# Performance work log

Hardware: AMD Instinct MI355X
Metric: run time of the kernel (lower is better)

## Reference

```python
import jax, jax.numpy as jnp
import numpy as np

KS = 3
N = KS * KS
LN_EPS = 1e-5


def conv2d(x, w, stride=1, pad=0):
    return jax.lax.conv_general_dilated(
        x, w, (stride, stride), [(pad, pad), (pad, pad)],
        dimension_numbers=('NCHW', 'OIHW', 'NCHW'))


def layer_norm(x, g, b):
    mu = jnp.mean(x, axis=-1, keepdims=True)
    var = jnp.mean(jnp.square(x - mu), axis=-1, keepdims=True)
    return (x - mu) * jax.lax.rsqrt(var + LN_EPS) * g + b


def l2norm(x):
    n = jnp.sqrt(jnp.sum(jnp.square(x), axis=-1, keepdims=True))
    return x / jnp.maximum(n, 1e-12)


def deform_conv(x, w_p, b_p, w_d):
    # canonical DeformConv2d (kernel 3, pad 1, stride 1, no modulation)
    B, C, H, W = x.shape
    off = conv2d(x, w_p, stride=1, pad=1) + b_p[None, :, None, None]  # [B,2N,H,W]
    xp = jnp.pad(x, ((0, 0), (0, 0), (1, 1), (1, 1)))
    Hp, Wp = H + 2, W + 2
    pn = jnp.stack(jnp.meshgrid(jnp.arange(-1, 2), jnp.arange(-1, 2), indexing='ij'), 0)
    pn = pn.reshape(2, N).astype(x.dtype)  # kernel offsets, row-major (dx,dy)
    p0x = jnp.arange(1, H + 1, dtype=x.dtype)
    p0y = jnp.arange(1, W + 1, dtype=x.dtype)
    # sampling coords, [B,H,W,N]
    px = off[:, :N].transpose(0, 2, 3, 1) + p0x[None, :, None, None] + pn[0][None, None, None, :]
    py = off[:, N:].transpose(0, 2, 3, 1) + p0y[None, None, :, None] + pn[1][None, None, None, :]
    fx = jnp.floor(px)
    fy = jnp.floor(py)
    qlx = jnp.clip(fx, 0, Hp - 1)
    qly = jnp.clip(fy, 0, Wp - 1)
    qrx = jnp.clip(fx + 1, 0, Hp - 1)
    qry = jnp.clip(fy + 1, 0, Wp - 1)
    pxc = jnp.clip(px, 0, Hp - 1)
    pyc = jnp.clip(py, 0, Wp - 1)
    g_lt = (1 + (qlx - pxc)) * (1 + (qly - pyc))
    g_rb = (1 - (qrx - pxc)) * (1 - (qry - pyc))
    g_lb = (1 + (qlx - pxc)) * (1 - (qry - pyc))
    g_rt = (1 - (qrx - pxc)) * (1 + (qly - pyc))
    xf = xp.reshape(B, C, Hp * Wp)

    def gat(ix, iy):
        idx = (ix.astype(jnp.int32) * Wp + iy.astype(jnp.int32)).reshape(B, 1, -1)
        g = jnp.take_along_axis(xf, jnp.broadcast_to(idx, (B, C, idx.shape[-1])), axis=2)
        return g.reshape(B, C, H, W, N)

    xo = (g_lt[:, None] * gat(qlx, qly) + g_rb[:, None] * gat(qrx, qry)
          + g_lb[:, None] * gat(qlx, qry) + g_rt[:, None] * gat(qrx, qly))
    # [B,C,H,W,N] -> [B,C,H*ks,W*ks] (row = h*ks+kr, col = w*ks+kc)
    xo = xo.reshape(B, C, H, W, KS, KS).transpose(0, 1, 2, 4, 3, 5).reshape(B, C, H * KS, W * KS)
    return conv2d(xo, w_d, stride=KS, pad=0)


def setup_inputs() -> dict:
    key = jax.random.key(0)
    ks = jax.random.split(key, 8)
    B, C, H, W, heads = 4, 192, 64, 64, 6
    hid = 4 * C
    return {
        'x': jax.random.normal(ks[0], (B, C, H, W), dtype=jnp.float32),
        'gamma1': jnp.ones((C,), jnp.float32),
        'beta1': jnp.zeros((C,), jnp.float32),
        'gamma2': jnp.ones((C,), jnp.float32),
        'beta2': jnp.zeros((C,), jnp.float32),
        'temperature': jnp.ones((heads, 1, 1), jnp.float32),
        'w_qkv': jax.random.normal(ks[1], (3 * C, C), jnp.float32) * 0.02,
        'w_proj': jax.random.normal(ks[2], (C, C), jnp.float32) * 0.02,
        'w_p': jax.random.normal(ks[3], (2 * N, C, KS, KS), jnp.float32) * 0.01,
        'b_p': jnp.zeros((2 * N,), jnp.float32),
        'w_d': jax.random.normal(ks[4], (C, C, KS, KS), jnp.float32) * 0.02,
        'w_fc1': jax.random.normal(ks[5], (C, hid), jnp.float32) * 0.02,
        'b_fc1': jnp.zeros((hid,), jnp.float32),
        'w_fc2': jax.random.normal(ks[6], (hid, C), jnp.float32) * 0.02,
        'b_fc2': jnp.zeros((C,), jnp.float32),
    }


def reference(x, gamma1, beta1, gamma2, beta2, temperature, w_qkv, w_proj,
              w_p, b_p, w_d, w_fc1, b_fc1, w_fc2, b_fc2):
    B, C, H, W = x.shape
    heads = temperature.shape[0]
    xs = x.reshape(B, C, H * W).transpose(0, 2, 1)  # [B,HW,C]
    shortcut = xs
    xn = layer_norm(xs, gamma1, beta1).transpose(0, 2, 1).reshape(B, C, H, W)
    # SSA: deformable-conv query + channel attention over C
    q = deform_conv(xn, w_p, b_p, w_d)
    qkv = jnp.einsum('bchw,oc->bohw', xn, w_qkv)
    k_spe, v_spe = qkv[:, C:2 * C], qkv[:, 2 * C:]

    def split(t):
        return t.reshape(B, heads, C // heads, H * W)

    qh = split(q)
    kh = l2norm(split(k_spe))
    vh = l2norm(split(v_spe))
    attn = jnp.einsum('bhcn,bhdn->bhcd', qh, kh) * temperature[None]
    attn = jax.nn.softmax(attn, axis=-1)
    out = jnp.einsum('bhcd,bhdn->bhcn', attn, vh).reshape(B, C, H, W)
    out = jnp.einsum('bchw,oc->bohw', out, w_proj)
    xs2 = shortcut + out.reshape(B, C, H * W).transpose(0, 2, 1)
    h1 = layer_norm(xs2, gamma2, beta2)
    m = jax.nn.gelu(h1 @ w_fc1 + b_fc1, approximate=False) @ w_fc2 + b_fc2
    xs3 = xs2 + m
    return xs3.transpose(0, 2, 1).reshape(B, C, H, W)
```

## Files before the change

### kernel.cpp

```cpp
#include <hip/hip_runtime.h>
#include <math.h>

typedef unsigned short u16;
typedef unsigned int u32;
typedef short s16x8 __attribute__((ext_vector_type(8)));
typedef float f32x4 __attribute__((ext_vector_type(4)));

#define AS1 __attribute__((address_space(1)))
#define AS3 __attribute__((address_space(3)))

__device__ __forceinline__ float bf2f(u16 u) {
    union { u32 i; float f; } v; v.i = ((u32)u) << 16; return v.f;
}
__device__ __forceinline__ u16 f2bf(float f) {
    union { float f; u32 i; } v; v.f = f;
    u32 r = v.i + 0x7fffu + ((v.i >> 16) & 1u);
    return (u16)(r >> 16);
}
__device__ __forceinline__ void gll16(const u16* g, u16* l) {
    __builtin_amdgcn_global_load_lds((const AS1 u32*)g, (AS3 u32*)l, 16, 0, 0);
}

__global__ void prep_kernel(const float* __restrict__ wd, const float* __restrict__ wqkv,
                            const float* __restrict__ wfc1, const float* __restrict__ wfc2,
                            const float* __restrict__ wp,
                            u16* __restrict__ wdT, u16* __restrict__ wkvT,
                            u16* __restrict__ wf1T, u16* __restrict__ wf2T,
                            u16* __restrict__ wpT)
{
    int i = blockIdx.x * 256 + threadIdx.x;
    if (i < 331776) {
        int o = i / 1728, r = i % 1728;
        int p = r / 192, c = r % 192;
        wdT[i] = f2bf(wd[(o * 192 + c) * 9 + p]);
    }
    if (i < 73728) {
        int o = i / 192, c = i % 192;
        wkvT[i] = f2bf(wqkv[(192 + o) * 192 + c]);
    }
    if (i < 147456) {
        int n = i / 192, c = i % 192;
        wf1T[i] = f2bf(wfc1[c * 768 + n]);
        int n2 = i / 768, hh = i % 768;
        wf2T[i] = f2bf(wfc2[hh * 192 + n2]);
    }
    if (i < 31104) {
        int n = i / 1728, r = i % 1728;
        int p = r / 192, c = r % 192;
        wpT[i] = f2bf(wp[(n * 192 + c) * 9 + p]);
    } else if (i < 55296) {
        wpT[i] = 0;
    }
}

__global__ __launch_bounds__(256) void ln1_kernel(const float* __restrict__ x,
                                                  const float* __restrict__ g,
                                                  const float* __restrict__ be,
                                                  u16* __restrict__ xn)
{
    __shared__ float red0[256], red1[256];
    __shared__ float mu_s[64], rs_s[64];
    __shared__ u16 tile[64 * 194];
    int t = threadIdx.x, tl = t & 63, cg = t >> 6;
    int m0 = blockIdx.x * 64;
    int b = m0 >> 12, hw0 = m0 & 4095;
    const float* xb = x + (size_t)b * 786432 + hw0 + tl;
    float s = 0.f, s2 = 0.f;
    for (int cc = cg; cc < 192; cc += 4) { float v = xb[cc * 4096]; s += v; s2 += v * v; }
    red0[t] = s; red1[t] = s2;
    __syncthreads();
    if (t < 64) {
        float a = red0[t] + red0[64 + t] + red0[128 + t] + red0[192 + t];
        float q = red1[t] + red1[64 + t] + red1[128 + t] + red1[192 + t];
        float mu = a * (1.f / 192.f);
        float var = q * (1.f / 192.f) - mu * mu;
        mu_s[t] = mu; rs_s[t] = rsqrtf(var + 1e-5f);
    }
    __syncthreads();
    float mu = mu_s[tl], rs = rs_s[tl];
    for (int cc = cg; cc < 192; cc += 4) {
        float v = (xb[cc * 4096] - mu) * rs * g[cc] + be[cc];
        tile[tl * 194 + cc] = f2bf(v);
    }
    __syncthreads();
    u32* dst = (u32*)(xn + (size_t)m0 * 192);
    for (int i = t; i < 64 * 96; i += 256) {
        int r = i / 96, c2 = i % 96;
        dst[i] = *(const u32*)&tile[r * 194 + c2 * 2];
    }
}

__global__ __launch_bounds__(256) void offconv_kernel(const u16* __restrict__ xn,
                                                      const u16* __restrict__ wpT,
                                                      const float* __restrict__ bp,
                                                      float* __restrict__ off)
{
    __shared__ u16 As[64 * 200];
    __shared__ u16 Bs[32 * 200];
    int bh = blockIdx.x;
    int b = bh >> 6, h = bh & 63;
    int t = threadIdx.x;
    int lane = t & 63, wv = t >> 6;
    f32x4 acc[2];
#pragma unroll
    for (int j = 0; j < 2; j++) { acc[j][0] = 0.f; acc[j][1] = 0.f; acc[j][2] = 0.f; acc[j][3] = 0.f; }
    int r = t >> 2, cq = (t & 3) * 48;
    for (int p = 0; p < 9; p++) {
        int dh = p / 3 - 1, dw = p % 3 - 1;
        int hr = h + dh, wr = r + dw;
        bool valid = (hr >= 0) && (hr < 64) && (wr >= 0) && (wr < 64);
        const u16* src = xn + ((size_t)(b * 4096 + hr * 64 + wr)) * 192 + cq;
#pragma unroll
        for (int j = 0; j < 6; j++) {
            s16x8 v = {0, 0, 0, 0, 0, 0, 0, 0};
            if (valid) v = *(const s16x8*)(src + j * 8);
            *(s16x8*)&As[r * 200 + cq + j * 8] = v;
        }
#pragma unroll
        for (int i = 0; i < 3; i++) {
            int q = t + i * 256;
            int n = q / 24, c8 = q % 24;
            *(s16x8*)&Bs[n * 200 + c8 * 8] =
                *(const s16x8*)(wpT + n * 1728 + p * 192 + c8 * 8);
        }
        __syncthreads();
#pragma unroll
        for (int kc = 0; kc < 6; kc++) {
            s16x8 af = *(const s16x8*)&As[(wv * 16 + (lane & 15)) * 200 + kc * 32 + (lane >> 4) * 8];
            s16x8 b0 = *(const s16x8*)&Bs[(lane & 15) * 200 + kc * 32 + (lane >> 4) * 8];
            s16x8 b1 = *(const s16x8*)&Bs[(16 + (lane & 15)) * 200 + kc * 32 + (lane >> 4) * 8];
            acc[0] = __builtin_amdgcn_mfma_f32_16x16x32_bf16(af, b0, acc[0], 0, 0, 0);
            acc[1] = __builtin_amdgcn_mfma_f32_16x16x32_bf16(af, b1, acc[1], 0, 0, 0);
        }
        __syncthreads();
    }
    int col = lane & 15;
    int wbase = wv * 16 + (lane >> 4) * 4;
#pragma unroll
    for (int j = 0; j < 2; j++) {
        int n = j * 16 + col;
        if (n < 18) {
            float bb = bp[n];
#pragma unroll
            for (int rr = 0; rr < 4; rr++) {
                int w = wbase + rr;
                off[((size_t)(b * 4096 + h * 64 + w)) * 18 + n] = acc[j][rr] + bb;
            }
        }
    }
}

__global__ __launch_bounds__(256) void gemm_deform(const u16* __restrict__ xn,
                                                   const float* __restrict__ off,
                                                   const u16* __restrict__ wdT,
                                                   u16* __restrict__ qt)
{
    __shared__ u16 As[2][32 * 200];
    __shared__ int sidx[32][9][4];
    __shared__ float swt[32][9][4];
    int t = threadIdx.x, lane = t & 63, wv = t >> 6;
    int m0 = blockIdx.x * 32;
    int b = m0 >> 12;
    for (int i = t; i < 288; i += 256) {
        int mi = i / 9, p = i % 9;
        int m = m0 + mi;
        int hw = m & 4095;
        int h = hw >> 6, w = hw & 63;
        float ox = off[(size_t)m * 18 + p];
        float oy = off[(size_t)m * 18 + 9 + p];
        float px = ox + (float)(h + 1) + (float)(p / 3 - 1);
        float py = oy + (float)(w + 1) + (float)(p % 3 - 1);
        float fx = floorf(px), fy = floorf(py);
        float qlx = fminf(fmaxf(fx, 0.f), 65.f);
        float qly = fminf(fmaxf(fy, 0.f), 65.f);
        float qrx = fminf(fmaxf(fx + 1.f, 0.f), 65.f);
        float qry = fminf(fmaxf(fy + 1.f, 0.f), 65.f);
        float pxc = fminf(fmaxf(px, 0.f), 65.f);
        float pyc = fminf(fmaxf(py, 0.f), 65.f);
        float gxl = 1.f + (qlx - pxc), gxr = 1.f - (qrx - pxc);
        float gyl = 1.f + (qly - pyc), gyr = 1.f - (qry - pyc);
        int xl = (int)qlx, xr = (int)qrx, yl = (int)qly, yr = (int)qry;
        int cx[4] = {xl, xr, xl, xr};
        int cy[4] = {yl, yr, yr, yl};
        float cw[4] = {gxl * gyl, gxr * gyr, gxl * gyr, gxr * gyl};
#pragma unroll
        for (int k = 0; k < 4; k++) {
            bool ok = (cx[k] >= 1) && (cx[k] <= 64) && (cy[k] >= 1) && (cy[k] <= 64);
            sidx[mi][p][k] = ok ? (b * 4096 + (cx[k] - 1) * 64 + (cy[k] - 1)) * 192 : 0;
            swt[mi][p][k] = ok ? cw[k] : 0.f;
        }
    }
    __syncthreads();
    f32x4 acc[2][3];
#pragma unroll
    for (int i = 0; i < 2; i++)
#pragma unroll
        for (int j = 0; j < 3; j++) {
            acc[i][j][0] = 0.f; acc[i][j][1] = 0.f; acc[i][j][2] = 0.f; acc[i][j][3] = 0.f;
        }
    int mi_[3], ch_[3];
#pragma unroll
    for (int u = 0; u < 3; u++) { int c = t + u * 256; mi_[u] = c / 24; ch_[u] = (c % 24) * 8; }

    {
        s16x8 pc[3][4];
#pragma unroll
        for (int u = 0; u < 3; u++) {
            const int* si = sidx[mi_[u]][0];
#pragma unroll
            for (int k = 0; k < 4; k++) pc[u][k] = *(const s16x8*)(xn + si[k] + ch_[u]);
        }
#pragma unroll
        for (int u = 0; u < 3; u++) {
            const float* sw = swt[mi_[u]][0];
            float v[8] = {0.f, 0.f, 0.f, 0.f, 0.f, 0.f, 0.f, 0.f};
#pragma unroll
            for (int k = 0; k < 4; k++) {
                float wt = sw[k];
#pragma unroll
                for (int j = 0; j < 8; j++) v[j] += wt * bf2f((u16)pc[u][k][j]);
            }
            s16x8 ov;
#pragma unroll
            for (int j = 0; j < 8; j++) ov[j] = (short)f2bf(v[j]);
            *(s16x8*)&As[0][mi_[u] * 200 + ch_[u]] = ov;
        }
    }
    __syncthreads();

    for (int p = 0; p < 9; p++) {
        int cur = p & 1;
        s16x8 nc[3][4];
        if (p < 8) {
#pragma unroll
            for (int u = 0; u < 3; u++) {
                const int* si = sidx[mi_[u]][p + 1];
#pragma unroll
                for (int k = 0; k < 4; k++) nc[u][k] = *(const s16x8*)(xn + si[k] + ch_[u]);
            }
        }
        const u16* wp_base = wdT + p * 192;
#pragma unroll
        for (int kk = 0; kk < 6; kk++) {
            s16x8 af[2], bfr[3];
#pragma unroll
            for (int i = 0; i < 2; i++)
                af[i] = *(const s16x8*)&As[cur][(i * 16 + (lane & 15)) * 200 + kk * 32 + (lane >> 4) * 8];
#pragma unroll
            for (int j = 0; j < 3; j++)
                bfr[j] = *(const s16x8*)(wp_base + (size_t)(wv * 48 + j * 16 + (lane & 15)) * 1728 + kk * 32 + (lane >> 4) * 8);
#pragma unroll
            for (int i = 0; i < 2; i++)
#pragma unroll
                for (int j = 0; j < 3; j++)
                    acc[i][j] = __builtin_amdgcn_mfma_f32_16x16x32_bf16(af[i], bfr[j], acc[i][j], 0, 0, 0);
        }
        if (p < 8) {
#pragma unroll
            for (int u = 0; u < 3; u++) {
                const float* sw = swt[mi_[u]][p + 1];
                float v[8] = {0.f, 0.f, 0.f, 0.f, 0.f, 0.f, 0.f, 0.f};
#pragma unroll
                for (int k = 0; k < 4; k++) {
                    float wt = sw[k];
#pragma unroll
                    for (int j = 0; j < 8; j++) v[j] += wt * bf2f((u16)nc[u][k][j]);
                }
                s16x8 ov;
#pragma unroll
                for (int j = 0; j < 8; j++) ov[j] = (short)f2bf(v[j]);
                *(s16x8*)&As[cur ^ 1][mi_[u] * 200 + ch_[u]] = ov;
            }
            __syncthreads();
        }
    }
    int col = lane & 15;
#pragma unroll
    for (int i = 0; i < 2; i++)
#pragma unroll
        for (int j = 0; j < 3; j++) {
            int mm = m0 + i * 16 + (lane >> 4) * 4;
            int nn = wv * 48 + j * 16 + col;
#pragma unroll
            for (int r = 0; r < 4; r++)
                qt[(size_t)(mm + r) * 192 + nn] = f2bf(acc[i][j][r]);
        }
}

template<int BM, int BN, int WM, int WN, int EP>
__global__ __launch_bounds__((BM / WM) * (BN / WN) * 64)
void gemm_bt(const u16* __restrict__ A, int lda,
             const u16* __restrict__ B, int ldb, int bstride,
             void* __restrict__ out, int ldc,
             const float* __restrict__ ex1, int K)
{
    constexpr int BK = 32;
    constexpr int WAVES_M = BM / WM, WAVES_N = BN / WN, NW = WAVES_M * WAVES_N;
    constexpr int TM = WM / 16, TN = WN / 16;
    constexpr int NLA = BM / 16, NLB = BN / 16;
    __shared__ u16 As[BM * BK];
    __shared__ u16 Bs[BN * BK];
    int tid = threadIdx.x;
    int lane = tid & 63, wv = tid >> 6;
    int wm = wv % WAVES_M, wn = wv / WAVES_M;
    int m0 = blockIdx.x * BM, n0 = blockIdx.y * BN;
    const u16* Bp = B + (size_t)(m0 >> 12) * bstride;
    f32x4 acc[TM][TN];
#pragma unroll
    for (int i = 0; i < TM; i++)
#pragma unroll
        for (int j = 0; j < TN; j++) {
            acc[i][j][0] = 0.f; acc[i][j][1] = 0.f; acc[i][j][2] = 0.f; acc[i][j][3] = 0.f;
        }
    int arow_l = lane >> 2;
    int acol_l = (lane & 3) * 8;
    for (int k0 = 0; k0 < K; k0 += BK) {
#pragma unroll 1
        for (int j = wv; j < NLA + NLB; j += NW) {
            if (j < NLA) {
                int row = j * 16 + arow_l;
                gll16(A + (size_t)(m0 + row) * lda + k0 + acol_l, As + j * 512);
            } else {
                int row = (j - NLA) * 16 + arow_l;
                gll16(Bp + (size_t)(n0 + row) * ldb + k0 + acol_l, Bs + (j - NLA) * 512);
            }
        }
        asm volatile("s_waitcnt vmcnt(0)" ::: "memory");
        __syncthreads();
        s16x8 af[TM], bfr[TN];
#pragma unroll
        for (int i = 0; i < TM; i++)
            af[i] = *(const s16x8*)&As[(wm * WM + i * 16 + (lane & 15)) * BK + (lane >> 4) * 8];
#pragma unroll
        for (int j = 0; j < TN; j++)
            bfr[j] = *(const s16x8*)&Bs[(wn * WN + j * 16 + (lane & 15)) * BK + (lane >> 4) * 8];
#pragma unroll
        for (int i = 0; i < TM; i++)
#pragma unroll
            for (int j = 0; j < TN; j++)
                acc[i][j] = __builtin_amdgcn_mfma_f32_16x16x32_bf16(af[i], bfr[j], acc[i][j], 0, 0, 0);
        __syncthreads();
    }
    int col = lane & 15;
#pragma unroll
    for (int i = 0; i < TM; i++)
#pragma unroll
        for (int j = 0; j < TN; j++) {
            int mm = m0 + wm * WM + i * 16 + (lane >> 4) * 4;
            int nn = n0 + wn * WN + j * 16 + col;
            if (EP == 0) {
                u16* o = (u16*)out;
#pragma unroll
                for (int r = 0; r < 4; r++) o[(size_t)(mm + r) * ldc + nn] = f2bf(acc[i][j][r]);
            } else if (EP == 1) {
                float* o = (float*)out;
                const float* xr = ex1 + (size_t)(mm >> 12) * 786432 + (size_t)nn * 4096 + (mm & 4095);
#pragma unroll
                for (int r = 0; r < 4; r++) o[(size_t)(mm + r) * ldc + nn] = acc[i][j][r] + xr[r];
            } else if (EP == 2) {
                u16* o = (u16*)out;
                float bb = ex1[nn];
#pragma unroll
                for (int r = 0; r < 4; r++) {
                    float v = acc[i][j][r] + bb;
                    o[(size_t)(mm + r) * ldc + nn] = f2bf(0.5f * v * (1.f + erff(v * 0.70710678118654752f)));
                }
            } else {
                float* o = (float*)out;
                float bb = ex1[nn];
#pragma unroll
                for (int r = 0; r < 4; r++) o[(size_t)(mm + r) * ldc + nn] = acc[i][j][r] + bb;
            }
        }
}

__global__ __launch_bounds__(384) void norm_kernel(const u16* __restrict__ kv,
                                                   float* __restrict__ norm2)
{
    int b = blockIdx.y, ch = blockIdx.x;
    int t = threadIdx.x;
    const u16* base = kv + ((size_t)(b * 4096 + ch * 128)) * 384 + t;
    float s = 0.f;
    for (int r = 0; r < 128; r++) { float v = bf2f(base[(size_t)r * 384]); s += v * v; }
    atomicAdd(&norm2[b * 384 + t], s);
}

__global__ __launch_bounds__(64) void attnp_kernel(const u16* __restrict__ qt,
                                                   const u16* __restrict__ kvt,
                                                   float* __restrict__ raw)
{
    __shared__ float qT[32 * 69];
    __shared__ float kT[32 * 69];
    int ch = blockIdx.x, h = blockIdx.y, b = blockIdx.z;
    int t = threadIdx.x;
    size_t base = (size_t)(b * 4096 + ch * 64);
    for (int e = t; e < 2048; e += 64) {
        int r = e >> 5, c = e & 31;
        qT[c * 69 + r] = bf2f(qt[(base + r) * 192 + h * 32 + c]);
        kT[c * 69 + r] = bf2f(kvt[(base + r) * 384 + h * 32 + c]);
    }
    __syncthreads();
    int tc = t >> 3, td = t & 7;
    int c0 = tc * 4, d0 = td * 4;
    float acc[4][4] = {};
    for (int r = 0; r < 64; r++) {
        float qv[4], kv4[4];
#pragma unroll
        for (int u = 0; u < 4; u++) { qv[u] = qT[(c0 + u) * 69 + r]; kv4[u] = kT[(d0 + u) * 69 + r]; }
#pragma unroll
        for (int u = 0; u < 4; u++)
#pragma unroll
            for (int v = 0; v < 4; v++) acc[u][v] += qv[u] * kv4[v];
    }
    float* dst = raw + ((size_t)(b * 6 + h)) * 1024;
#pragma unroll
    for (int u = 0; u < 4; u++)
#pragma unroll
        for (int v = 0; v < 4; v++)
            atomicAdd(&dst[(c0 + u) * 32 + d0 + v], acc[u][v]);
}

__global__ __launch_bounds__(1024) void softmax_kernel(const float* __restrict__ raw,
                                                       const float* __restrict__ norm2,
                                                       const float* __restrict__ temp,
                                                       float* __restrict__ att2)
{
    int h = blockIdx.x, b = blockIdx.y;
    int t = threadIdx.x;
    int c = t >> 5, d = t & 31;
    __shared__ float invk[32], invv[32];
    if (t < 32)       invk[t] = 1.f / fmaxf(sqrtf(norm2[b * 384 + h * 32 + t]), 1e-12f);
    else if (t < 64)  invv[t - 32] = 1.f / fmaxf(sqrtf(norm2[b * 384 + 192 + h * 32 + (t - 32)]), 1e-12f);
    __syncthreads();
    float T = temp[h];
    float v = raw[((size_t)(b * 6 + h) * 32 + c) * 32 + d] * invk[d] * T;
    float mx = v;
    for (int s = 16; s > 0; s >>= 1) mx = fmaxf(mx, __shfl_xor(mx, s, 32));
    float e = expf(v - mx);
    float sm = e;
    for (int s = 16; s > 0; s >>= 1) sm += __shfl_xor(sm, s, 32);
    att2[((size_t)(b * 6 + h) * 32 + c) * 32 + d] = (e / sm) * invv[d];
}

__global__ __launch_bounds__(192) void mb_kernel(const float* __restrict__ wproj,
                                                 const float* __restrict__ att2,
                                                 u16* __restrict__ Mb)
{
    int o2 = blockIdx.x, b = blockIdx.y, t = threadIdx.x;
    int h = t >> 5, d = t & 31;
    float s = 0.f;
#pragma unroll
    for (int c = 0; c < 32; c++)
        s += wproj[o2 * 192 + h * 32 + c] * att2[((size_t)(b * 6 + h) * 32 + c) * 32 + d];
    Mb[((size_t)b * 192 + o2) * 192 + t] = f2bf(s);
}

__global__ __launch_bounds__(256) void ln2_kernel(const float* __restrict__ xs2,
                                                  const float* __restrict__ g,
                                                  const float* __restrict__ be,
                                                  u16* __restrict__ h1)
{
    int t = threadIdx.x;
    int wv = t >> 6, l = t & 63;
    size_t m = (size_t)blockIdx.x * 4 + wv;
    const float* row = xs2 + m * 192;
    float v0 = row[l], v1 = row[l + 64], v2 = row[l + 128];
    float s = v0 + v1 + v2, s2 = v0 * v0 + v1 * v1 + v2 * v2;
    for (int sh = 32; sh > 0; sh >>= 1) { s += __shfl_xor(s, sh); s2 += __shfl_xor(s2, sh); }
    float mu = s * (1.f / 192.f);
    float var = s2 * (1.f / 192.f) - mu * mu;
    float rs = rsqrtf(var + 1e-5f);
    u16* o = h1 + m * 192;
    o[l]       = f2bf((v0 - mu) * rs * g[l]       + be[l]);
    o[l + 64]  = f2bf((v1 - mu) * rs * g[l + 64]  + be[l + 64]);
    o[l + 128] = f2bf((v2 - mu) * rs * g[l + 128] + be[l + 128]);
}

__global__ __launch_bounds__(256) void final_kernel(const float* __restrict__ xs2,
                                                    const float* __restrict__ m2,
                                                    float* __restrict__ out)
{
    __shared__ float tile[192 * 65];
    int blk = blockIdx.x;
    int b = blk >> 6, hw0 = (blk & 63) * 64;
    int t = threadIdx.x;
    size_t mbase = ((size_t)b * 4096 + hw0) * 192;
    for (int i = t; i < 64 * 192; i += 256) {
        int r = i / 192, c = i % 192;
        tile[c * 65 + r] = xs2[mbase + i] + m2[mbase + i];
    }
    __syncthreads();
    for (int i = t; i < 64 * 192; i += 256) {
        int c = i / 64, r = i % 64;
        out[(size_t)b * 786432 + (size_t)c * 4096 + hw0 + r] = tile[c * 65 + r];
    }
}

extern "C" void kernel_launch(void* const* d_in, const int* in_sizes, int n_in,
                              void* d_out, int out_size, void* d_ws, size_t ws_size,
                              hipStream_t stream)
{
    const float* x      = (const float*)d_in[0];
    const float* gamma1 = (const float*)d_in[1];
    const float* beta1  = (const float*)d_in[2];
    const float* gamma2 = (const float*)d_in[3];
    const float* beta2  = (const float*)d_in[4];
    const float* temp   = (const float*)d_in[5];
    const float* w_qkv  = (const float*)d_in[6];
    const float* w_proj = (const float*)d_in[7];
    const float* w_p    = (const float*)d_in[8];
    const float* b_p    = (const float*)d_in[9];
    const float* w_d    = (const float*)d_in[10];
    const float* w_fc1  = (const float*)d_in[11];
    const float* b_fc1  = (const float*)d_in[12];
    const float* w_fc2  = (const float*)d_in[13];
    const float* b_fc2  = (const float*)d_in[14];
    float* out = (float*)d_out;
    char* ws = (char*)d_ws;

    u16*   xn    = (u16*)(ws + 0);
    float* off   = (float*)(ws + 6291456);
    u16*   adef  = (u16*)(ws + 7471104);
    u16*   wpT   = adef;
    u16*   m1    = adef;
    float* m2    = (float*)(ws + 7471104 + 25165824);
    u16*   qt    = (u16*)(ws + 64094208);
    u16*   kvt   = (u16*)(ws + 70385664);
    float* norm2 = (float*)(ws + 82968576);
    float* araw  = (float*)(ws + 82974720);
    float* att2  = (float*)(ws + 83073024);
    u16*   Mb    = (u16*)(ws + 83171328);
    float* xs2   = (float*)(ws + 83318784);
    u16*   h1    = xn;
    u16*   wdT   = (u16*)(ws + 95901696);
    u16*   wkvT  = (u16*)(ws + 96565248);
    u16*   wf1T  = (u16*)(ws + 96712704);
    u16*   wf2T  = (u16*)(ws + 97007616);

    hipMemsetAsync(norm2, 0, 6144 + 98304, stream);
    prep_kernel<<<1296, 256, 0, stream>>>(w_d, w_qkv, w_fc1, w_fc2, w_p, wdT, wkvT, wf1T, wf2T, wpT);
    ln1_kernel<<<256, 256, 0, stream>>>(x, gamma1, beta1, xn);
    offconv_kernel<<<256, 256, 0, stream>>>(xn, wpT, b_p, off);
    gemm_deform<<<512, 256, 0, stream>>>(xn, off, wdT, qt);
    gemm_bt<128, 128, 64, 64, 0><<<dim3(128, 3), 256, 0, stream>>>(xn, 192, wkvT, 192, 0, kvt, 384, nullptr, 192);
    norm_kernel<<<dim3(32, 4), 384, 0, stream>>>(kvt, norm2);
    attnp_kernel<<<dim3(64, 6, 4), 64, 0, stream>>>(qt, kvt, araw);
    softmax_kernel<<<dim3(6, 4), 1024, 0, stream>>>(araw, norm2, temp, att2);
    mb_kernel<<<dim3(192, 4), 192, 0, stream>>>(w_proj, att2, Mb);
    gemm_bt<32, 192, 32, 96, 1><<<dim3(512, 1), 128, 0, stream>>>(kvt + 192, 384, Mb, 192, 192 * 192, xs2, 192, x, 192);
    ln2_kernel<<<4096, 256, 0, stream>>>(xs2, gamma2, beta2, h1);
    gemm_bt<128, 128, 64, 64, 2><<<dim3(128, 6), 256, 0, stream>>>(h1, 192, wf1T, 192, 0, m1, 768, b_fc1, 192);
    gemm_bt<32, 192, 32, 96, 3><<<dim3(512, 1), 128, 0, stream>>>(m1, 768, wf2T, 768, 0, m2, 192, b_fc2, 768);
    final_kernel<<<256, 256, 0, stream>>>(xs2, m2, out);
}
```

Before: 292.4 us.

## Double deform-GEMM block threads and split waves across M and N tiles

The deformable-conv GEMM kernel now runs 512 threads per block as 8 waves arranged 2x4 over M and N. Each wave computes a 16x48 tile instead of 32x48, and each thread gathers 12 channels of one sample point with 12-byte vector loads instead of three 8-channel chunks. The aim is more wave-level parallelism and fewer live registers per thread, to hide the latency of the scattered bilinear gathers. In exchange the same weight fragments are loaded from global memory by twice as many waves, and the 12-byte loads are less aligned.

```diff
diff --git a/kernel.cpp b/kernel.cpp
--- a/kernel.cpp
+++ b/kernel.cpp
@@ -5,12 +5,19 @@
 typedef unsigned int u32;
 typedef short s16x8 __attribute__((ext_vector_type(8)));
 typedef float f32x4 __attribute__((ext_vector_type(4)));
+typedef u32 u32x3 __attribute__((ext_vector_type(3)));
 
 #define AS1 __attribute__((address_space(1)))
 #define AS3 __attribute__((address_space(3)))
 
 __device__ __forceinline__ float bf2f(u16 u) {
     union { u32 i; float f; } v; v.i = ((u32)u) << 16; return v.f;
+}
+__device__ __forceinline__ float bflo(u32 u) {
+    union { u32 i; float f; } v; v.i = u << 16; return v.f;
+}
+__device__ __forceinline__ float bfhi(u32 u) {
+    union { u32 i; float f; } v; v.i = u & 0xffff0000u; return v.f;
 }
 __device__ __forceinline__ u16 f2bf(float f) {
     union { float f; u32 i; } v; v.f = f;
@@ -150,18 +157,19 @@
     }
 }
 
-__global__ __launch_bounds__(256) void gemm_deform(const u16* __restrict__ xn,
-                                                   const float* __restrict__ off,
-                                                   const u16* __restrict__ wdT,
-                                                   u16* __restrict__ qt)
+__global__ __launch_bounds__(512, 4) void gemm_deform(const u16* __restrict__ xn,
+                                                      const float* __restrict__ off,
+                                                      const u16* __restrict__ wdT,
+                                                      u16* __restrict__ qt)
 {
     __shared__ u16 As[2][32 * 200];
     __shared__ int sidx[32][9][4];
     __shared__ float swt[32][9][4];
     int t = threadIdx.x, lane = t & 63, wv = t >> 6;
+    int wm = wv & 1, wn = wv >> 1;
     int m0 = blockIdx.x * 32;
     int b = m0 >> 12;
-    for (int i = t; i < 288; i += 256) {
+    for (int i = t; i < 288; i += 512) {
         int mi = i / 9, p = i % 9;
         int m = m0 + mi;
         int hw = m & 4095;
@@ -191,100 +199,96 @@
         }
     }
     __syncthreads();
-    f32x4 acc[2][3];
-#pragma unroll
-    for (int i = 0; i < 2; i++)
-#pragma unroll
-        for (int j = 0; j < 3; j++) {
-            acc[i][j][0] = 0.f; acc[i][j][1] = 0.f; acc[i][j][2] = 0.f; acc[i][j][3] = 0.f;
-        }
-    int mi_[3], ch_[3];
-#pragma unroll
-    for (int u = 0; u < 3; u++) { int c = t + u * 256; mi_[u] = c / 24; ch_[u] = (c % 24) * 8; }
+    f32x4 acc[3];
+#pragma unroll
+    for (int j = 0; j < 3; j++) { acc[j][0] = 0.f; acc[j][1] = 0.f; acc[j][2] = 0.f; acc[j][3] = 0.f; }
+    int mi = t >> 4, ch = (t & 15) * 12;
 
     {
-        s16x8 pc[3][4];
-#pragma unroll
-        for (int u = 0; u < 3; u++) {
-            const int* si = sidx[mi_[u]][0];
-#pragma unroll
-            for (int k = 0; k < 4; k++) pc[u][k] = *(const s16x8*)(xn + si[k] + ch_[u]);
-        }
-#pragma unroll
-        for (int u = 0; u < 3; u++) {
-            const float* sw = swt[mi_[u]][0];
-            float v[8] = {0.f, 0.f, 0.f, 0.f, 0.f, 0.f, 0.f, 0.f};
+        const int*   si = sidx[mi][0];
+        const float* sw = swt[mi][0];
+        float v[12];
+#pragma unroll
+        for (int j = 0; j < 12; j++) v[j] = 0.f;
+#pragma unroll
+        for (int k = 0; k < 4; k++) {
+            u32x3 a = *(const u32x3*)(xn + si[k] + ch);
+            u32x3 c2 = *(const u32x3*)(xn + si[k] + ch + 6);
+            float wt = sw[k];
+#pragma unroll
+            for (int j = 0; j < 3; j++) {
+                v[2 * j]     += wt * bflo(a[j]);
+                v[2 * j + 1] += wt * bfhi(a[j]);
+                v[6 + 2 * j]     += wt * bflo(c2[j]);
+                v[6 + 2 * j + 1] += wt * bfhi(c2[j]);
+            }
+        }
+        u32 o[6];
+#pragma unroll
+        for (int j = 0; j < 6; j++)
+            o[j] = (u32)f2bf(v[2 * j]) | ((u32)f2bf(v[2 * j + 1]) << 16);
+        *(u32x3*)&As[0][mi * 200 + ch]     = u32x3{o[0], o[1], o[2]};
+        *(u32x3*)&As[0][mi * 200 + ch + 6] = u32x3{o[3], o[4], o[5]};
+    }
+    __syncthreads();
+
+    for (int p = 0; p < 9; p++) {
+        int cur = p & 1;
+        u32x3 na[4], nb[4];
+        if (p < 8) {
+            const int* si = sidx[mi][p + 1];
+#pragma unroll
+            for (int k = 0; k < 4; k++) {
+                na[k] = *(const u32x3*)(xn + si[k] + ch);
+                nb[k] = *(const u32x3*)(xn + si[k] + ch + 6);
+            }
+        }
+        const u16* wp_base = wdT + p * 192;
+#pragma unroll
+        for (int kk = 0; kk < 6; kk++) {
+            s16x8 af = *(const s16x8*)&As[cur][(wm * 16 + (lane & 15)) * 200 + kk * 32 + (lane >> 4) * 8];
+            s16x8 bfr[3];
+#pragma unroll
+            for (int j = 0; j < 3; j++)
+                bfr[j] = *(const s16x8*)(wp_base + (size_t)(wn * 48 + j * 16 + (lane & 15)) * 1728 + kk * 32 + (lane >> 4) * 8);
+#pragma unroll
+            for (int j = 0; j < 3; j++)
+                acc[j] = __builtin_amdgcn_mfma_f32_16x16x32_bf16(af, bfr[j], acc[j], 0, 0, 0);
+        }
+        if (p < 8) {
+            const float* sw = swt[mi][p + 1];
+            float v[12];
+#pragma unroll
+            for (int j = 0; j < 12; j++) v[j] = 0.f;
 #pragma unroll
             for (int k = 0; k < 4; k++) {
                 float wt = sw[k];
 #pragma unroll
-                for (int j = 0; j < 8; j++) v[j] += wt * bf2f((u16)pc[u][k][j]);
+                for (int j = 0; j < 3; j++) {
+                    v[2 * j]     += wt * bflo(na[k][j]);
+                    v[2 * j + 1] += wt * bfhi(na[k][j]);
+                    v[6 + 2 * j]     += wt * bflo(nb[k][j]);
+                    v[6 + 2 * j + 1] += wt * bfhi(nb[k][j]);
+                }
             }
-            s16x8 ov;
-#pragma unroll
-            for (int j = 0; j < 8; j++) ov[j] = (short)f2bf(v[j]);
-            *(s16x8*)&As[0][mi_[u] * 200 + ch_[u]] = ov;
-        }
-    }
-    __syncthreads();
-
-    for (int p = 0; p < 9; p++) {
-        int cur = p & 1;
-        s16x8 nc[3][4];
-        if (p < 8) {
-#pragma unroll
-            for (int u = 0; u < 3; u++) {
-                const int* si = sidx[mi_[u]][p + 1];
-#pragma unroll
-                for (int k = 0; k < 4; k++) nc[u][k] = *(const s16x8*)(xn + si[k] + ch_[u]);
-            }
-        }
-        const u16* wp_base = wdT + p * 192;
-#pragma unroll
-        for (int kk = 0; kk < 6; kk++) {
-            s16x8 af[2], bfr[3];
-#pragma unroll
-            for (int i = 0; i < 2; i++)
-                af[i] = *(const s16x8*)&As[cur][(i * 16 + (lane & 15)) * 200 + kk * 32 + (lane >> 4) * 8];
-#pragma unroll
-            for (int j = 0; j < 3; j++)
-                bfr[j] = *(const s16x8*)(wp_base + (size_t)(wv * 48 + j * 16 + (lane & 15)) * 1728 + kk * 32 + (lane >> 4) * 8);
-#pragma unroll
-            for (int i = 0; i < 2; i++)
-#pragma unroll
-                for (int j = 0; j < 3; j++)
-                    acc[i][j] = __builtin_amdgcn_mfma_f32_16x16x32_bf16(af[i], bfr[j], acc[i][j], 0, 0, 0);
-        }
-        if (p < 8) {
-#pragma unroll
-            for (int u = 0; u < 3; u++) {
-                const float* sw = swt[mi_[u]][p + 1];
-                float v[8] = {0.f, 0.f, 0.f, 0.f, 0.f, 0.f, 0.f, 0.f};
-#pragma unroll
-                for (int k = 0; k < 4; k++) {
-                    float wt = sw[k];
-#pragma unroll
-                    for (int j = 0; j < 8; j++) v[j] += wt * bf2f((u16)nc[u][k][j]);
-                }
-                s16x8 ov;
-#pragma unroll
-                for (int j = 0; j < 8; j++) ov[j] = (short)f2bf(v[j]);
-                *(s16x8*)&As[cur ^ 1][mi_[u] * 200 + ch_[u]] = ov;
-            }
+            u32 o[6];
+#pragma unroll
+            for (int j = 0; j < 6; j++)
+                o[j] = (u32)f2bf(v[2 * j]) | ((u32)f2bf(v[2 * j + 1]) << 16);
+            *(u32x3*)&As[cur ^ 1][mi * 200 + ch]     = u32x3{o[0], o[1], o[2]};
+            *(u32x3*)&As[cur ^ 1][mi * 200 + ch + 6] = u32x3{o[3], o[4], o[5]};
             __syncthreads();
         }
     }
     int col = lane & 15;
 #pragma unroll
-    for (int i = 0; i < 2; i++)
-#pragma unroll
-        for (int j = 0; j < 3; j++) {
-            int mm = m0 + i * 16 + (lane >> 4) * 4;
-            int nn = wv * 48 + j * 16 + col;
-#pragma unroll
-            for (int r = 0; r < 4; r++)
-                qt[(size_t)(mm + r) * 192 + nn] = f2bf(acc[i][j][r]);
-        }
+    for (int j = 0; j < 3; j++) {
+        int mm = m0 + wm * 16 + (lane >> 4) * 4;
+        int nn = wn * 48 + j * 16 + col;
+#pragma unroll
+        for (int r = 0; r < 4; r++)
+            qt[(size_t)(mm + r) * 192 + nn] = f2bf(acc[j][r]);
+    }
 }
 
 template<int BM, int BN, int WM, int WN, int EP>
@@ -541,7 +545,7 @@
     prep_kernel<<<1296, 256, 0, stream>>>(w_d, w_qkv, w_fc1, w_fc2, w_p, wdT, wkvT, wf1T, wf2T, wpT);
     ln1_kernel<<<256, 256, 0, stream>>>(x, gamma1, beta1, xn);
     offconv_kernel<<<256, 256, 0, stream>>>(xn, wpT, b_p, off);
-    gemm_deform<<<512, 256, 0, stream>>>(xn, off, wdT, qt);
+    gemm_deform<<<512, 512, 0, stream>>>(xn, off, wdT, qt);
     gemm_bt<128, 128, 64, 64, 0><<<dim3(128, 3), 256, 0, stream>>>(xn, 192, wkvT, 192, 0, kvt, 384, nullptr, 192);
     norm_kernel<<<dim3(32, 4), 384, 0, stream>>>(kvt, norm2);
     attnp_kernel<<<dim3(64, 6, 4), 64, 0, stream>>>(qt, kvt, araw);
```

Result: slower. 330.6 us (+13.0%).

## Stage deform-conv weight slices in swizzled LDS with a larger M tile

Applied to the files above, without the earlier changes.

The deform GEMM now works on 64-row tiles with 512 threads and 8 waves arranged 2x4. For each kernel tap it loads the full 192x192 weight slice into LDS via global_load_lds, in an XOR-swizzled layout produced by the prep kernel, so B fragments come from shared memory instead of strided global reads. The double-buffered A tile becomes a single buffer with an extra barrier. This cuts repeated global weight traffic per block but raises LDS use to about 100KB, which limits occupancy, and it serializes the weight load with compute.

```diff
diff --git a/kernel.cpp b/kernel.cpp
--- a/kernel.cpp
+++ b/kernel.cpp
@@ -32,7 +32,8 @@
     if (i < 331776) {
         int o = i / 1728, r = i % 1728;
         int p = r / 192, c = r % 192;
-        wdT[i] = f2bf(wd[(o * 192 + c) * 9 + p]);
+        int cs = c ^ ((o & 7) << 3);
+        wdT[(p * 192 + o) * 192 + cs] = f2bf(wd[(o * 192 + c) * 9 + p]);
     }
     if (i < 73728) {
         int o = i / 192, c = i % 192;
@@ -150,18 +151,20 @@
     }
 }
 
-__global__ __launch_bounds__(256) void gemm_deform(const u16* __restrict__ xn,
-                                                   const float* __restrict__ off,
-                                                   const u16* __restrict__ wdT,
-                                                   u16* __restrict__ qt)
-{
-    __shared__ u16 As[2][32 * 200];
-    __shared__ int sidx[32][9][4];
-    __shared__ float swt[32][9][4];
+__global__ __launch_bounds__(512, 2) void gemm_deform(const u16* __restrict__ xn,
+                                                      const float* __restrict__ off,
+                                                      const u16* __restrict__ wdT,
+                                                      u16* __restrict__ qt)
+{
+    __shared__ u16 As[64 * 200];
+    __shared__ u16 Bs[192 * 192];
+    __shared__ int sidx[64][9][4];
+    __shared__ float swt[64][9][4];
     int t = threadIdx.x, lane = t & 63, wv = t >> 6;
-    int m0 = blockIdx.x * 32;
+    int wm = wv & 1, wn = wv >> 1;
+    int m0 = blockIdx.x * 64;
     int b = m0 >> 12;
-    for (int i = t; i < 288; i += 256) {
+    for (int i = t; i < 576; i += 512) {
         int mi = i / 9, p = i % 9;
         int m = m0 + mi;
         int hw = m & 4095;
@@ -198,79 +201,103 @@
         for (int j = 0; j < 3; j++) {
             acc[i][j][0] = 0.f; acc[i][j][1] = 0.f; acc[i][j][2] = 0.f; acc[i][j][3] = 0.f;
         }
-    int mi_[3], ch_[3];
-#pragma unroll
-    for (int u = 0; u < 3; u++) { int c = t + u * 256; mi_[u] = c / 24; ch_[u] = (c % 24) * 8; }
+    int mi = t >> 3, ch = (t & 7) * 24;
+    int orow[3], oxr[3];
+#pragma unroll
+    for (int j = 0; j < 3; j++) {
+        int o = wn * 48 + j * 16 + (lane & 15);
+        orow[j] = o * 192;
+        oxr[j] = (o & 7) << 3;
+    }
+    int kb0 = (lane >> 4) * 8;
 
     {
-        s16x8 pc[3][4];
-#pragma unroll
-        for (int u = 0; u < 3; u++) {
-            const int* si = sidx[mi_[u]][0];
-#pragma unroll
-            for (int k = 0; k < 4; k++) pc[u][k] = *(const s16x8*)(xn + si[k] + ch_[u]);
-        }
-#pragma unroll
-        for (int u = 0; u < 3; u++) {
-            const float* sw = swt[mi_[u]][0];
-            float v[8] = {0.f, 0.f, 0.f, 0.f, 0.f, 0.f, 0.f, 0.f};
+        const u16* bsrc = wdT;
+#pragma unroll
+        for (int i2 = 0; i2 < 9; i2++) {
+            int jc = wv + 8 * i2;
+            gll16(bsrc + jc * 512 + lane * 8, Bs + jc * 512);
+        }
+        const int*   si = sidx[mi][0];
+        const float* sw = swt[mi][0];
+        s16x8 pc[4][3];
+#pragma unroll
+        for (int k = 0; k < 4; k++)
+#pragma unroll
+            for (int s = 0; s < 3; s++)
+                pc[k][s] = *(const s16x8*)(xn + si[k] + ch + s * 8);
+        float v[24];
+#pragma unroll
+        for (int j = 0; j < 24; j++) v[j] = 0.f;
+#pragma unroll
+        for (int k = 0; k < 4; k++) {
+            float wt = sw[k];
+#pragma unroll
+            for (int j = 0; j < 24; j++) v[j] += wt * bf2f((u16)pc[k][j >> 3][j & 7]);
+        }
+#pragma unroll
+        for (int s = 0; s < 3; s++) {
+            s16x8 ov;
+#pragma unroll
+            for (int e = 0; e < 8; e++) ov[e] = (short)f2bf(v[s * 8 + e]);
+            *(s16x8*)&As[mi * 200 + ch + s * 8] = ov;
+        }
+        asm volatile("s_waitcnt vmcnt(0)" ::: "memory");
+        __syncthreads();
+    }
+
+    for (int p = 0; p < 9; p++) {
+        s16x8 nc[4][3];
+        if (p < 8) {
+            const int* si = sidx[mi][p + 1];
+#pragma unroll
+            for (int k = 0; k < 4; k++)
+#pragma unroll
+                for (int s = 0; s < 3; s++)
+                    nc[k][s] = *(const s16x8*)(xn + si[k] + ch + s * 8);
+        }
+#pragma unroll
+        for (int kk = 0; kk < 6; kk++) {
+            int kb = kk * 32 + kb0;
+            s16x8 af[2], bfr[3];
+#pragma unroll
+            for (int i = 0; i < 2; i++)
+                af[i] = *(const s16x8*)&As[(wm * 32 + i * 16 + (lane & 15)) * 200 + kb];
+#pragma unroll
+            for (int j = 0; j < 3; j++)
+                bfr[j] = *(const s16x8*)&Bs[orow[j] + (kb ^ oxr[j])];
+#pragma unroll
+            for (int i = 0; i < 2; i++)
+#pragma unroll
+                for (int j = 0; j < 3; j++)
+                    acc[i][j] = __builtin_amdgcn_mfma_f32_16x16x32_bf16(af[i], bfr[j], acc[i][j], 0, 0, 0);
+        }
+        if (p < 8) {
+            __syncthreads();
+            const u16* bsrc = wdT + (size_t)(p + 1) * 36864;
+#pragma unroll
+            for (int i2 = 0; i2 < 9; i2++) {
+                int jc = wv + 8 * i2;
+                gll16(bsrc + jc * 512 + lane * 8, Bs + jc * 512);
+            }
+            const float* sw = swt[mi][p + 1];
+            float v[24];
+#pragma unroll
+            for (int j = 0; j < 24; j++) v[j] = 0.f;
 #pragma unroll
             for (int k = 0; k < 4; k++) {
                 float wt = sw[k];
 #pragma unroll
-                for (int j = 0; j < 8; j++) v[j] += wt * bf2f((u16)pc[u][k][j]);
+                for (int j = 0; j < 24; j++) v[j] += wt * bf2f((u16)nc[k][j >> 3][j & 7]);
             }
-            s16x8 ov;
-#pragma unroll
-            for (int j = 0; j < 8; j++) ov[j] = (short)f2bf(v[j]);
-            *(s16x8*)&As[0][mi_[u] * 200 + ch_[u]] = ov;
-        }
-    }
-    __syncthreads();
-
-    for (int p = 0; p < 9; p++) {
-        int cur = p & 1;
-        s16x8 nc[3][4];
-        if (p < 8) {
-#pragma unroll
-            for (int u = 0; u < 3; u++) {
-                const int* si = sidx[mi_[u]][p + 1];
-#pragma unroll
-                for (int k = 0; k < 4; k++) nc[u][k] = *(const s16x8*)(xn + si[k] + ch_[u]);
+#pragma unroll
+            for (int s = 0; s < 3; s++) {
+                s16x8 ov;
+#pragma unroll
+                for (int e = 0; e < 8; e++) ov[e] = (short)f2bf(v[s * 8 + e]);
+                *(s16x8*)&As[mi * 200 + ch + s * 8] = ov;
             }
-        }
-        const u16* wp_base = wdT + p * 192;
-#pragma unroll
-        for (int kk = 0; kk < 6; kk++) {
-            s16x8 af[2], bfr[3];
-#pragma unroll
-            for (int i = 0; i < 2; i++)
-                af[i] = *(const s16x8*)&As[cur][(i * 16 + (lane & 15)) * 200 + kk * 32 + (lane >> 4) * 8];
-#pragma unroll
-            for (int j = 0; j < 3; j++)
-                bfr[j] = *(const s16x8*)(wp_base + (size_t)(wv * 48 + j * 16 + (lane & 15)) * 1728 + kk * 32 + (lane >> 4) * 8);
-#pragma unroll
-            for (int i = 0; i < 2; i++)
-#pragma unroll
-                for (int j = 0; j < 3; j++)
-                    acc[i][j] = __builtin_amdgcn_mfma_f32_16x16x32_bf16(af[i], bfr[j], acc[i][j], 0, 0, 0);
-        }
-        if (p < 8) {
-#pragma unroll
-            for (int u = 0; u < 3; u++) {
-                const float* sw = swt[mi_[u]][p + 1];
-                float v[8] = {0.f, 0.f, 0.f, 0.f, 0.f, 0.f, 0.f, 0.f};
-#pragma unroll
-                for (int k = 0; k < 4; k++) {
-                    float wt = sw[k];
-#pragma unroll
-                    for (int j = 0; j < 8; j++) v[j] += wt * bf2f((u16)nc[u][k][j]);
-                }
-                s16x8 ov;
-#pragma unroll
-                for (int j = 0; j < 8; j++) ov[j] = (short)f2bf(v[j]);
-                *(s16x8*)&As[cur ^ 1][mi_[u] * 200 + ch_[u]] = ov;
-            }
+            asm volatile("s_waitcnt vmcnt(0)" ::: "memory");
             __syncthreads();
         }
     }
@@ -279,8 +306,8 @@
     for (int i = 0; i < 2; i++)
 #pragma unroll
         for (int j = 0; j < 3; j++) {
-            int mm = m0 + i * 16 + (lane >> 4) * 4;
-            int nn = wv * 48 + j * 16 + col;
+            int mm = m0 + wm * 32 + i * 16 + (lane >> 4) * 4;
+            int nn = wn * 48 + j * 16 + col;
 #pragma unroll
             for (int r = 0; r < 4; r++)
                 qt[(size_t)(mm + r) * 192 + nn] = f2bf(acc[i][j][r]);
@@ -541,7 +568,7 @@
     prep_kernel<<<1296, 256, 0, stream>>>(w_d, w_qkv, w_fc1, w_fc2, w_p, wdT, wkvT, wf1T, wf2T, wpT);
     ln1_kernel<<<256, 256, 0, stream>>>(x, gamma1, beta1, xn);
     offconv_kernel<<<256, 256, 0, stream>>>(xn, wpT, b_p, off);
-    gemm_deform<<<512, 256, 0, stream>>>(xn, off, wdT, qt);
+    gemm_deform<<<256, 512, 0, stream>>>(xn, off, wdT, qt);
     gemm_bt<128, 128, 64, 64, 0><<<dim3(128, 3), 256, 0, stream>>>(xn, 192, wkvT, 192, 0, kvt, 384, nullptr, 192);
     norm_kernel<<<dim3(32, 4), 384, 0, stream>>>(kvt, norm2);
     attnp_kernel<<<dim3(64, 6, 4), 64, 0, stream>>>(qt, kvt, araw);
```

New measurement: 272.6 us. 1.07x faster.
